# Performance work log

Hardware: AMD Instinct MI355X
Metric: run time of the kernel (lower is better)

The kernel has to match this reference:

```python
import jax, jax.numpy as jnp
import numpy as np

DIM, HEADS, K = 64, 4, 7
HEAD_DIM = DIM // HEADS
SCALE = HEAD_DIM ** -0.5  # qk_scale = head_dim ** -0.5


def setup_inputs() -> dict:
    key = jax.random.key(0)
    ks = jax.random.split(key, 6)
    B, H, W, SH, SW = 1, 192, 192, 12, 12
    x = jax.random.normal(ks[0], (B, DIM, H, W), dtype=jnp.float32)
    # soft pixel->superpixel association probabilities in [0,1)
    sims = jax.random.uniform(ks[1], (B, H, W, SH, SW), dtype=jnp.float32)
    s = DIM ** -0.5
    w_q = jax.random.normal(ks[2], (DIM, DIM), dtype=jnp.float32) * s
    w_k = jax.random.normal(ks[3], (DIM, DIM), dtype=jnp.float32) * s
    w_v = jax.random.normal(ks[4], (DIM, DIM), dtype=jnp.float32) * s
    w_proj = jax.random.normal(ks[5], (DIM, DIM), dtype=jnp.float32) * s
    return {"x": x, "sims": sims, "w_q": w_q, "w_k": w_k, "w_v": w_v, "w_proj": w_proj}


def _forward(x, sims, w_q, w_k, w_v, w_proj):
    B, C, H, W = x.shape
    SH, SW = sims.shape[-2:]
    h, d = HEADS, C // HEADS
    xf = jnp.transpose(x, (0, 2, 3, 1))                 # [B,H,W,C]
    q = (xf @ w_q).reshape(B, H, W, h, d)
    k = (xf @ w_k).reshape(B, H, W, h, d)
    v = (xf @ w_v).reshape(B, H, W, h, d)
    # NATTEN-style clamped neighborhood window starts
    sy = jnp.clip(jnp.arange(H) - K // 2, 0, H - K)     # [H]
    sx = jnp.clip(jnp.arange(W) - K // 2, 0, W - K)     # [W]
    # get_indices: nearest-interp of superpixel label grid -> hard cell per pixel
    si = (jnp.arange(H) * SH) // H                      # [H]
    sj = (jnp.arange(W) * SW) // W                      # [W]
    logits, masks = [], []
    for ky in range(K):                                  # fixed small kernel loop
        ny = sy + ky
        for kx in range(K):
            nx = sx + kx
            k_n = k[:, ny][:, :, nx]                    # [B,H,W,h,d] gathered neighbor keys
            logits.append(jnp.einsum('byxhd,byxhd->bhyx', q, k_n))
            # prob. neighbor pixel j belongs to query pixel i's superpixel cell
            masks.append(sims[:, ny[:, None], nx[None, :], si[:, None], sj[None, :]])  # [B,H,W]
    logits = jnp.stack(logits, -1)                      # [B,h,H,W,K*K]
    mask = jnp.stack(masks, -1)[:, None]                # [B,1,H,W,K*K]
    attn = jax.nn.softmax(SCALE * logits * mask, axis=-1)
    attn_m = attn * mask                                # soft-mask weighted aggregation
    out = jnp.zeros((B, h, H, W, d), x.dtype)
    o = 0
    for ky in range(K):
        ny = sy + ky
        for kx in range(K):
            nx = sx + kx
            v_n = jnp.transpose(v[:, ny][:, :, nx], (0, 3, 1, 2, 4))  # [B,h,H,W,d]
            out = out + attn_m[..., o, None] * v_n
            o += 1
    out = jnp.transpose(out, (0, 2, 3, 1, 4)).reshape(B, H, W, C)
    out = out @ w_proj
    return jnp.transpose(out, (0, 3, 1, 2))             # back to NCHW


def reference(x, sims, w_q, w_k, w_v, w_proj):
    return _forward(x, sims, w_q, w_k, w_v, w_proj)
```

## Files before the change

### kernel.cpp

```cpp
#include <hip/hip_runtime.h>
#include <math.h>

#define HH 192
#define WW 192
#define NPIX (HH * WW)
#define SCALE 0.25f

#define HLY 14
#define HLX 10
#define NH  (HLY * HLX)
#define REG2 (NH * 8 + 4)

typedef __attribute__((ext_vector_type(8))) _Float16 f16x8;
typedef __attribute__((ext_vector_type(2))) _Float16 f16x2;
typedef __attribute__((ext_vector_type(4))) float f32x4;

#if __has_builtin(__builtin_amdgcn_fdot2)
#define FDOT2(a, b, c) __builtin_amdgcn_fdot2((a), (b), (c), false)
#else
#define FDOT2(a, b, c) fmaf((float)(a)[0], (float)(b)[0], \
                            fmaf((float)(a)[1], (float)(b)[1], (c)))
#endif

static __device__ __forceinline__ f16x2 u2h(unsigned int u)
{
    f16x2 r; __builtin_memcpy(&r, &u, 4); return r;
}

static __device__ __forceinline__ short f16s(float f)
{
    _Float16 h = (_Float16)f;
    short s; __builtin_memcpy(&s, &h, 2); return s;
}

static __device__ __forceinline__ unsigned int pack_f16(float a, float b)
{
    unsigned short ul = (unsigned short)f16s(a);
    unsigned short uh = (unsigned short)f16s(b);
    return ((unsigned int)uh << 16) | ul;
}

__global__ __launch_bounds__(256) void qkv_mfma(
    const float* __restrict__ x,
    const float* __restrict__ wq, const float* __restrict__ wk,
    const float* __restrict__ wv, const float* __restrict__ wp,
    unsigned int* __restrict__ qg, unsigned int* __restrict__ kg,
    unsigned int* __restrict__ vg, short* __restrict__ wT)
{
    const int t = threadIdx.x;

    if (blockIdx.x == NPIX / 64) {
        #pragma unroll
        for (int i = 0; i < 16; ++i) {
            const int idx = i * 256 + t;
            const int n = idx >> 6, k = idx & 63;
            wT[(192 + n) * 64 + k] = f16s(wp[k * 64 + n]);
        }
        return;
    }

    __shared__ short lds[(64 + 192) * 72];
    short* xT = lds;
    short* wTs = lds + 64 * 72;
    const int px0 = blockIdx.x * 64;

    #pragma unroll
    for (int r = 0; r < 16; ++r) {
        const int idx = r * 256 + t;
        const int cin = idx >> 6, pxl = idx & 63;
        xT[pxl * 72 + cin] = f16s(x[(size_t)cin * NPIX + px0 + pxl]);
    }
    #pragma unroll
    for (int m = 0; m < 3; ++m) {
        const float* ws = (m == 0) ? wq : (m == 1) ? wk : wv;
        #pragma unroll
        for (int r = 0; r < 16; ++r) {
            const int idx = r * 256 + t;
            const int k = idx >> 6, n = idx & 63;
            wTs[(m * 64 + n) * 72 + k] = f16s(ws[k * 64 + n]);
        }
    }
    __syncthreads();

    const int lane = t & 63;
    const int wid  = t >> 6;
    const int l15  = lane & 15;
    const int kg4  = lane >> 4;

    f32x4 acc[12];
    #pragma unroll
    for (int nt = 0; nt < 12; ++nt) acc[nt] = (f32x4){0.f, 0.f, 0.f, 0.f};

    #pragma unroll
    for (int ks = 0; ks < 2; ++ks) {
        const f16x8 a = *reinterpret_cast<const f16x8*>(
            &xT[(wid * 16 + l15) * 72 + ks * 32 + kg4 * 8]);
        #pragma unroll
        for (int nt = 0; nt < 12; ++nt) {
            const f16x8 b = *reinterpret_cast<const f16x8*>(
                &wTs[(nt * 16 + l15) * 72 + ks * 32 + kg4 * 8]);
            acc[nt] = __builtin_amdgcn_mfma_f32_16x16x32_f16(a, b, acc[nt], 0, 0, 0);
        }
    }

    #pragma unroll
    for (int nt = 0; nt < 12; ++nt) {
        unsigned int* dst = (nt < 4) ? qg : (nt < 8) ? kg : vg;
        const int dwb = (nt & 3) * 8 + (l15 >> 1);
        #pragma unroll
        for (int r = 0; r < 4; ++r) {
            const float val = acc[nt][r];
            const float par = __shfl_xor(val, 1, 64);
            if (!(lane & 1)) {
                const int opx = px0 + wid * 16 + kg4 * 4 + r;
                dst[(size_t)opx * 32 + dwb] = pack_f16(val, par);
            }
        }
    }
}

#define NBR_STEP(HIDX)                                                        \
    {                                                                         \
        const int hidx_ = (HIDX);                                             \
        const uint4 ka = *reinterpret_cast<const uint4*>(kreg + hidx_ * 8);   \
        const uint4 k2 = *reinterpret_cast<const uint4*>(kreg + hidx_ * 8 + 4);\
        float da = FDOT2(u2h(ka.x), qv2[0], 0.f);                             \
        float db = FDOT2(u2h(ka.y), qv2[1], 0.f);                             \
        da = FDOT2(u2h(ka.z), qv2[2], da);                                    \
        db = FDOT2(u2h(ka.w), qv2[3], db);                                    \
        da = FDOT2(u2h(k2.x), qv2[4], da);                                    \
        db = FDOT2(u2h(k2.y), qv2[5], db);                                    \
        da = FDOT2(u2h(k2.z), qv2[6], da);                                    \
        db = FDOT2(u2h(k2.w), qv2[7], db);                                    \
        const float dot = da + db;                                            \
        const float m = sm[hidx_];                                            \
        const float pf = __expf(SCALE * dot * m) * 0.0625f;                   \
        S += pf;                                                              \
        const _Float16 pmh = (_Float16)(pf * m);                              \
        const f16x2 pm2 = {pmh, pmh};                                         \
        const uint4 va = *reinterpret_cast<const uint4*>(vreg + hidx_ * 8);   \
        const uint4 v2 = *reinterpret_cast<const uint4*>(vreg + hidx_ * 8 + 4);\
        acc2[0] = pm2 * u2h(va.x) + acc2[0];                                  \
        acc2[1] = pm2 * u2h(va.y) + acc2[1];                                  \
        acc2[2] = pm2 * u2h(va.z) + acc2[2];                                  \
        acc2[3] = pm2 * u2h(va.w) + acc2[3];                                  \
        acc2[4] = pm2 * u2h(v2.x) + acc2[4];                                  \
        acc2[5] = pm2 * u2h(v2.y) + acc2[5];                                  \
        acc2[6] = pm2 * u2h(v2.z) + acc2[6];                                  \
        acc2[7] = pm2 * u2h(v2.w) + acc2[7];                                  \
    }

__global__ __launch_bounds__(256) void attn_proj(
    const unsigned int* __restrict__ qg,
    const unsigned int* __restrict__ kg,
    const unsigned int* __restrict__ vg,
    const float* __restrict__ sims,
    const short* __restrict__ wT,
    float* __restrict__ out)
{
    __shared__ unsigned int smem[8 * REG2 + NH];

    const int bid = blockIdx.x;
    const int tl = (bid & 7) * 144 + (bid >> 3);
    const int ty = tl / 48, tx = tl - ty * 48;
    const int Y0 = ty * 8, X0 = tx * 4;
    int hy0 = Y0 - 3; hy0 = hy0 < 0 ? 0 : (hy0 > HH - HLY ? HH - HLY : hy0);
    int hx0 = X0 - 3; hx0 = hx0 < 0 ? 0 : (hx0 > WW - HLX ? WW - HLX : hx0);
    const int t = threadIdx.x;

    #pragma unroll
    for (int i = 0; i < 5; ++i) {
        const int idx = i * 256 + t;
        if (idx < NH * 8) {
            const int hidx = idx >> 3, u = idx & 7;
            const int r = hidx / HLX, c = hidx - r * HLX;
            const int np = (hy0 + r) * WW + hx0 + c;
            const int h = u >> 1, hf = u & 1;
            const size_t src = (size_t)np * 32 + u * 4;
            const uint4 kk = *reinterpret_cast<const uint4*>(kg + src);
            const uint4 vv = *reinterpret_cast<const uint4*>(vg + src);
            unsigned int* dk = smem + h * REG2 + hidx * 8 + hf * 4;
            *reinterpret_cast<uint4*>(dk) = kk;
            *reinterpret_cast<uint4*>(dk + 4 * REG2) = vv;
        }
    }
    if (t < NH) {
        const int r = t / HLX, c = t - r * HLX;
        const int np = (hy0 + r) * WW + hx0 + c;
        const int sbase = (Y0 >> 4) * 12 + (X0 >> 4);
        reinterpret_cast<float*>(smem)[8 * REG2 + t] = sims[np * 144 + sbase];
    }
    __syncthreads();

    const int half = t & 1, hl = (t >> 1) & 1, p = (t >> 2) & 31, hp = t >> 7;
    const int h = hp * 2 + hl;
    const int py = p >> 2, pxq = p & 3;
    const int y = Y0 + py, xq = X0 + pxq;
    int sy = y - 3;  sy = sy < 0 ? 0 : (sy > HH - 7 ? HH - 7 : sy);
    int sx = xq - 3; sx = sx < 0 ? 0 : (sx > WW - 7 ? WW - 7 : sx);
    const int wbase = (sy - hy0) * HLX + (sx - hx0);

    f16x2 qv2[8];
    {
        const unsigned int* qp = qg + (size_t)(y * WW + xq) * 32 + h * 8;
        const uint4 a = *reinterpret_cast<const uint4*>(qp);
        const uint4 b = *reinterpret_cast<const uint4*>(qp + 4);
        qv2[0] = u2h(a.x); qv2[1] = u2h(a.y); qv2[2] = u2h(a.z); qv2[3] = u2h(a.w);
        qv2[4] = u2h(b.x); qv2[5] = u2h(b.y); qv2[6] = u2h(b.z); qv2[7] = u2h(b.w);
    }

    const unsigned int* kreg = smem + h * REG2;
    const unsigned int* vreg = smem + (4 + h) * REG2;
    const float* sm = reinterpret_cast<const float*>(smem + 8 * REG2);

    float S = 0.f;
    f16x2 acc2[8];
    #pragma unroll
    for (int d = 0; d < 8; ++d) acc2[d] = (f16x2){(_Float16)0.f, (_Float16)0.f};

    #pragma unroll
    for (int i = 0; i < 24; ++i) {
        const int nn = 2 * i + half;
        const int ky = (nn * 37) >> 8;
        const int kx = nn - 7 * ky;
        NBR_STEP(wbase + ky * HLX + kx);
    }
    if (half == 0) {
        NBR_STEP(wbase + 6 * HLX + 6);
    }

    const float S2 = S + __shfl_xor(S, 1, 64);
    float lo[8], hi[8];
    #pragma unroll
    for (int j = 0; j < 8; ++j) {
        lo[j] = (float)acc2[j >> 1][j & 1];
        hi[j] = (float)acc2[4 + (j >> 1)][j & 1];
    }
    #pragma unroll
    for (int j = 0; j < 8; ++j) {
        lo[j] += __shfl_xor(lo[j], 1, 64);
        hi[j] += __shfl_xor(hi[j], 1, 64);
    }
    const float inv = 1.f / S2;
    float o[8];
    #pragma unroll
    for (int j = 0; j < 8; ++j) o[j] = ((half == 0) ? lo[j] : hi[j]) * inv;

    __syncthreads();
    {
        short* A_lds = reinterpret_cast<short*>(smem);
        const uint4 w4 = make_uint4(pack_f16(o[0], o[1]), pack_f16(o[2], o[3]),
                                    pack_f16(o[4], o[5]), pack_f16(o[6], o[7]));
        *reinterpret_cast<uint4*>(&A_lds[p * 72 + h * 16 + half * 8]) = w4;
    }
    __syncthreads();

    const short* A_lds = reinterpret_cast<const short*>(smem);
    const int lane = t & 63;
    const int w    = t >> 6;
    const int mt   = w & 1;
    const int np2  = w >> 1;
    const int l15  = lane & 15;
    const int kg4  = lane >> 4;

    f16x8 afrag[2];
    #pragma unroll
    for (int ks = 0; ks < 2; ++ks)
        afrag[ks] = *reinterpret_cast<const f16x8*>(
            &A_lds[(mt * 16 + l15) * 72 + ks * 32 + kg4 * 8]);

    #pragma unroll
    for (int nt2 = 0; nt2 < 2; ++nt2) {
        const int nt = np2 * 2 + nt2;
        const int n = nt * 16 + l15;
        f32x4 pacc = (f32x4){0.f, 0.f, 0.f, 0.f};
        #pragma unroll
        for (int ks = 0; ks < 2; ++ks) {
            const f16x8 b = *reinterpret_cast<const f16x8*>(
                &wT[(192 + n) * 64 + ks * 32 + kg4 * 8]);
            pacc = __builtin_amdgcn_mfma_f32_16x16x32_f16(afrag[ks], b, pacc, 0, 0, 0);
        }
        const int pr = mt * 16 + kg4 * 4;
        const int gy = Y0 + (pr >> 2);
        *reinterpret_cast<float4*>(out + (size_t)n * NPIX + gy * WW + X0) =
            make_float4(pacc[0], pacc[1], pacc[2], pacc[3]);
    }
}

extern "C" void kernel_launch(void* const* d_in, const int* in_sizes, int n_in,
                              void* d_out, int out_size, void* d_ws, size_t ws_size,
                              hipStream_t stream)
{
    const float* x    = (const float*)d_in[0];
    const float* sims = (const float*)d_in[1];
    const float* wq   = (const float*)d_in[2];
    const float* wk   = (const float*)d_in[3];
    const float* wv   = (const float*)d_in[4];
    const float* wp   = (const float*)d_in[5];
    float* out = (float*)d_out;

    unsigned int* qg = (unsigned int*)d_ws;
    unsigned int* kg = qg + (size_t)NPIX * 32;
    unsigned int* vg = kg + (size_t)NPIX * 32;
    short* wT = (short*)(vg + (size_t)NPIX * 32);

    qkv_mfma<<<NPIX / 64 + 1, 256, 0, stream>>>(x, wq, wk, wv, wp, qg, kg, vg, wT);
    attn_proj<<<1152, 256, 0, stream>>>(qg, kg, vg, sims, wT, out);
}
```

Measured before the change: 38.48 us.

## Compute neighborhood attention with MFMA over dense halo tile using transpose LDS reads

Replaces the per-thread fdot2 neighborhood loop with MFMA matrix products. Each wave, one per head, computes QK scores for 16 queries against a 10x16 halo of keys and applies PV with another MFMA, masking out-of-window entries. The tile shape changes to 4x8, V is staged in LDS and read with ds_read_b64_tr_b16, K is loaded straight from global, and exp is folded into exp2 with a prescaled mask. This trades redundant dense computation over about 160 slots per query against the 49 needed for far higher matrix throughput. It also depends on inline asm and a hand-placed waitcnt.

```diff
diff --git a/kernel.cpp b/kernel.cpp
--- a/kernel.cpp
+++ b/kernel.cpp
@@ -5,27 +5,24 @@
 #define WW 192
 #define NPIX (HH * WW)
 #define SCALE 0.25f
-
-#define HLY 14
-#define HLX 10
-#define NH  (HLY * HLX)
-#define REG2 (NH * 8 + 4)
+#define C1 0.36067376f
+
+#define HR 10
+#define HC 14
+#define NSLOT 160
+#define VOFF 160
 
 typedef __attribute__((ext_vector_type(8))) _Float16 f16x8;
-typedef __attribute__((ext_vector_type(2))) _Float16 f16x2;
+typedef __attribute__((ext_vector_type(4))) _Float16 f16x4;
 typedef __attribute__((ext_vector_type(4))) float f32x4;
 
-#if __has_builtin(__builtin_amdgcn_fdot2)
-#define FDOT2(a, b, c) __builtin_amdgcn_fdot2((a), (b), (c), false)
+#if __has_builtin(__builtin_amdgcn_exp2f)
+#define EXP2(x) __builtin_amdgcn_exp2f(x)
 #else
-#define FDOT2(a, b, c) fmaf((float)(a)[0], (float)(b)[0], \
-                            fmaf((float)(a)[1], (float)(b)[1], (c)))
+#define EXP2(x) exp2f(x)
 #endif
 
-static __device__ __forceinline__ f16x2 u2h(unsigned int u)
-{
-    f16x2 r; __builtin_memcpy(&r, &u, 4); return r;
-}
+#define MFMA16(a, b, c) __builtin_amdgcn_mfma_f32_16x16x16f16((a), (b), (c), 0, 0, 0)
 
 static __device__ __forceinline__ short f16s(float f)
 {
@@ -119,37 +116,6 @@
     }
 }
 
-#define NBR_STEP(HIDX)                                                        \
-    {                                                                         \
-        const int hidx_ = (HIDX);                                             \
-        const uint4 ka = *reinterpret_cast<const uint4*>(kreg + hidx_ * 8);   \
-        const uint4 k2 = *reinterpret_cast<const uint4*>(kreg + hidx_ * 8 + 4);\
-        float da = FDOT2(u2h(ka.x), qv2[0], 0.f);                             \
-        float db = FDOT2(u2h(ka.y), qv2[1], 0.f);                             \
-        da = FDOT2(u2h(ka.z), qv2[2], da);                                    \
-        db = FDOT2(u2h(ka.w), qv2[3], db);                                    \
-        da = FDOT2(u2h(k2.x), qv2[4], da);                                    \
-        db = FDOT2(u2h(k2.y), qv2[5], db);                                    \
-        da = FDOT2(u2h(k2.z), qv2[6], da);                                    \
-        db = FDOT2(u2h(k2.w), qv2[7], db);                                    \
-        const float dot = da + db;                                            \
-        const float m = sm[hidx_];                                            \
-        const float pf = __expf(SCALE * dot * m) * 0.0625f;                   \
-        S += pf;                                                              \
-        const _Float16 pmh = (_Float16)(pf * m);                              \
-        const f16x2 pm2 = {pmh, pmh};                                         \
-        const uint4 va = *reinterpret_cast<const uint4*>(vreg + hidx_ * 8);   \
-        const uint4 v2 = *reinterpret_cast<const uint4*>(vreg + hidx_ * 8 + 4);\
-        acc2[0] = pm2 * u2h(va.x) + acc2[0];                                  \
-        acc2[1] = pm2 * u2h(va.y) + acc2[1];                                  \
-        acc2[2] = pm2 * u2h(va.z) + acc2[2];                                  \
-        acc2[3] = pm2 * u2h(va.w) + acc2[3];                                  \
-        acc2[4] = pm2 * u2h(v2.x) + acc2[4];                                  \
-        acc2[5] = pm2 * u2h(v2.y) + acc2[5];                                  \
-        acc2[6] = pm2 * u2h(v2.z) + acc2[6];                                  \
-        acc2[7] = pm2 * u2h(v2.w) + acc2[7];                                  \
-    }
-
 __global__ __launch_bounds__(256) void attn_proj(
     const unsigned int* __restrict__ qg,
     const unsigned int* __restrict__ kg,
@@ -158,110 +124,144 @@
     const short* __restrict__ wT,
     float* __restrict__ out)
 {
-    __shared__ unsigned int smem[8 * REG2 + NH];
+    __shared__ unsigned int smem[VOFF + 4 * 160 * 8];
 
     const int bid = blockIdx.x;
     const int tl = (bid & 7) * 144 + (bid >> 3);
-    const int ty = tl / 48, tx = tl - ty * 48;
-    const int Y0 = ty * 8, X0 = tx * 4;
-    int hy0 = Y0 - 3; hy0 = hy0 < 0 ? 0 : (hy0 > HH - HLY ? HH - HLY : hy0);
-    int hx0 = X0 - 3; hx0 = hx0 < 0 ? 0 : (hx0 > WW - HLX ? WW - HLX : hx0);
+    const int ty = tl / 24, tx = tl - ty * 24;
+    const int Y0 = ty * 4, X0 = tx * 8;
+    int hy0 = Y0 - 3; hy0 = hy0 < 0 ? 0 : (hy0 > HH - HR ? HH - HR : hy0);
+    int hx0 = X0 - 3; hx0 = hx0 < 0 ? 0 : (hx0 > WW - HC ? WW - HC : hx0);
     const int t = threadIdx.x;
 
     #pragma unroll
     for (int i = 0; i < 5; ++i) {
         const int idx = i * 256 + t;
-        if (idx < NH * 8) {
-            const int hidx = idx >> 3, u = idx & 7;
-            const int r = hidx / HLX, c = hidx - r * HLX;
-            const int np = (hy0 + r) * WW + hx0 + c;
-            const int h = u >> 1, hf = u & 1;
-            const size_t src = (size_t)np * 32 + u * 4;
-            const uint4 kk = *reinterpret_cast<const uint4*>(kg + src);
-            const uint4 vv = *reinterpret_cast<const uint4*>(vg + src);
-            unsigned int* dk = smem + h * REG2 + hidx * 8 + hf * 4;
-            *reinterpret_cast<uint4*>(dk) = kk;
-            *reinterpret_cast<uint4*>(dk + 4 * REG2) = vv;
-        }
-    }
-    if (t < NH) {
-        const int r = t / HLX, c = t - r * HLX;
-        const int np = (hy0 + r) * WW + hx0 + c;
-        const int sbase = (Y0 >> 4) * 12 + (X0 >> 4);
-        reinterpret_cast<float*>(smem)[8 * REG2 + t] = sims[np * 144 + sbase];
+        const int n = idx >> 3, u = idx & 7;
+        const int ry = n >> 4, cx = n & 15;
+        uint4 vv = make_uint4(0u, 0u, 0u, 0u);
+        if (cx < HC) {
+            const int np = (hy0 + ry) * WW + hx0 + cx;
+            vv = *reinterpret_cast<const uint4*>(vg + (size_t)np * 32 + u * 4);
+        }
+        const int h = u >> 1, hf = u & 1;
+        *reinterpret_cast<uint4*>(smem + VOFF + h * 1280 + n * 8 + hf * 4) = vv;
+    }
+    if (t < NSLOT) {
+        const int ry = t >> 4, cx = t & 15;
+        float m = 0.f;
+        if (cx < HC) {
+            const int np = (hy0 + ry) * WW + hx0 + cx;
+            const int sbase = (Y0 >> 4) * 12 + (X0 >> 4);
+            m = sims[np * 144 + sbase];
+        }
+        reinterpret_cast<float*>(smem)[t] = m * C1;
     }
     __syncthreads();
 
-    const int half = t & 1, hl = (t >> 1) & 1, p = (t >> 2) & 31, hp = t >> 7;
-    const int h = hp * 2 + hl;
-    const int py = p >> 2, pxq = p & 3;
-    const int y = Y0 + py, xq = X0 + pxq;
-    int sy = y - 3;  sy = sy < 0 ? 0 : (sy > HH - 7 ? HH - 7 : sy);
-    int sx = xq - 3; sx = sx < 0 ? 0 : (sx > WW - 7 ? WW - 7 : sx);
-    const int wbase = (sy - hy0) * HLX + (sx - hx0);
-
-    f16x2 qv2[8];
-    {
-        const unsigned int* qp = qg + (size_t)(y * WW + xq) * 32 + h * 8;
-        const uint4 a = *reinterpret_cast<const uint4*>(qp);
-        const uint4 b = *reinterpret_cast<const uint4*>(qp + 4);
-        qv2[0] = u2h(a.x); qv2[1] = u2h(a.y); qv2[2] = u2h(a.z); qv2[3] = u2h(a.w);
-        qv2[4] = u2h(b.x); qv2[5] = u2h(b.y); qv2[6] = u2h(b.z); qv2[7] = u2h(b.w);
-    }
-
-    const unsigned int* kreg = smem + h * REG2;
-    const unsigned int* vreg = smem + (4 + h) * REG2;
-    const float* sm = reinterpret_cast<const float*>(smem + 8 * REG2);
-
-    float S = 0.f;
-    f16x2 acc2[8];
-    #pragma unroll
-    for (int d = 0; d < 8; ++d) acc2[d] = (f16x2){(_Float16)0.f, (_Float16)0.f};
-
-    #pragma unroll
-    for (int i = 0; i < 24; ++i) {
-        const int nn = 2 * i + half;
-        const int ky = (nn * 37) >> 8;
-        const int kx = nn - 7 * ky;
-        NBR_STEP(wbase + ky * HLX + kx);
-    }
-    if (half == 0) {
-        NBR_STEP(wbase + 6 * HLX + 6);
-    }
-
-    const float S2 = S + __shfl_xor(S, 1, 64);
-    float lo[8], hi[8];
-    #pragma unroll
-    for (int j = 0; j < 8; ++j) {
-        lo[j] = (float)acc2[j >> 1][j & 1];
-        hi[j] = (float)acc2[4 + (j >> 1)][j & 1];
-    }
-    #pragma unroll
-    for (int j = 0; j < 8; ++j) {
-        lo[j] += __shfl_xor(lo[j], 1, 64);
-        hi[j] += __shfl_xor(hi[j], 1, 64);
-    }
-    const float inv = 1.f / S2;
-    float o[8];
-    #pragma unroll
-    for (int j = 0; j < 8; ++j) o[j] = ((half == 0) ? lo[j] : hi[j]) * inv;
+    const int h    = t >> 6;
+    const int lane = t & 63;
+    const int l15  = lane & 15;
+    const int kg4  = lane >> 4;
+    const float* mC = reinterpret_cast<const float*>(smem);
+
+    const unsigned vbyte = (unsigned)(uintptr_t)smem + VOFF * 4
+                         + h * 5120 + lane * 8;
+    f16x4 vf[10];
+#define TRREAD(I, IMM) \
+    asm volatile("ds_read_b64_tr_b16 %0, %1 offset:" IMM \
+                 : "=v"(vf[I]) : "v"(vbyte))
+    TRREAD(0, "0");    TRREAD(1, "512");  TRREAD(2, "1024"); TRREAD(3, "1536");
+    TRREAD(4, "2048"); TRREAD(5, "2560"); TRREAD(6, "3072"); TRREAD(7, "3584");
+    TRREAD(8, "4096"); TRREAD(9, "4608");
+#undef TRREAD
+
+    const unsigned int* kgp = kg + (size_t)(hy0 * WW + hx0 + l15) * 32
+                            + h * 8 + kg4 * 2;
+    f16x4 kf[10];
+    #pragma unroll
+    for (int nt = 0; nt < 10; ++nt)
+        kf[nt] = *reinterpret_cast<const f16x4*>(kgp + (size_t)nt * (WW * 32));
+
+    f32x4 oacc[2];
+    float invq[2];
+    bool waited = false;
+
+    #pragma unroll
+    for (int qt = 0; qt < 2; ++qt) {
+        const int q = qt * 16 + l15;
+        const int qry = q >> 3, qcx = q & 7;
+        const int y = Y0 + qry, x = X0 + qcx;
+        int sy = y - 3; sy = sy < 0 ? 0 : (sy > HH - 7 ? HH - 7 : sy);
+        int sx = x - 3; sx = sx < 0 ? 0 : (sx > WW - 7 ? WW - 7 : sx);
+        const int wy = sy - hy0, wx = sx - hx0;
+
+        const f16x4 qb = *reinterpret_cast<const f16x4*>(
+            qg + (size_t)(y * WW + x) * 32 + h * 8 + kg4 * 2);
+
+        f32x4 s[10];
+        #pragma unroll
+        for (int nt = 0; nt < 10; ++nt)
+            s[nt] = MFMA16(kf[nt], qb, ((f32x4){0.f, 0.f, 0.f, 0.f}));
+
+        float vx[4];
+        #pragma unroll
+        for (int rr = 0; rr < 4; ++rr)
+            vx[rr] = ((unsigned)(kg4 * 4 + rr - wx) < 7u) ? 1.f : 0.f;
+
+        float Ss = 0.f;
+        f16x4 pt[10];
+        #pragma unroll
+        for (int nt = 0; nt < 10; ++nt) {
+            const f32x4 mcv = *reinterpret_cast<const f32x4*>(
+                mC + nt * 16 + kg4 * 4);
+            const float vy = ((unsigned)(nt - wy) < 7u) ? 1.f : 0.f;
+            float pf[4];
+            #pragma unroll
+            for (int e = 0; e < 4; ++e) {
+                const float u = s[nt][e] * mcv[e];
+                const float p = EXP2(u);
+                const float pv = p * vy * vx[e];
+                Ss += pv;
+                pf[e] = pv * mcv[e];
+            }
+            pt[nt] = (f16x4){(_Float16)pf[0], (_Float16)pf[1],
+                             (_Float16)pf[2], (_Float16)pf[3]};
+        }
+        Ss += __shfl_xor(Ss, 16, 64);
+        Ss += __shfl_xor(Ss, 32, 64);
+        invq[qt] = 1.f / (C1 * Ss);
+
+        if (!waited) {
+            asm volatile("s_waitcnt lgkmcnt(0)" ::: "memory");
+            __builtin_amdgcn_sched_barrier(0);
+            waited = true;
+        }
+        f32x4 o = (f32x4){0.f, 0.f, 0.f, 0.f};
+        #pragma unroll
+        for (int nt = 0; nt < 10; ++nt)
+            o = MFMA16(vf[nt], pt[nt], o);
+        oacc[qt] = o;
+    }
 
     __syncthreads();
     {
-        short* A_lds = reinterpret_cast<short*>(smem);
-        const uint4 w4 = make_uint4(pack_f16(o[0], o[1]), pack_f16(o[2], o[3]),
-                                    pack_f16(o[4], o[5]), pack_f16(o[6], o[7]));
-        *reinterpret_cast<uint4*>(&A_lds[p * 72 + h * 16 + half * 8]) = w4;
+        short* A = reinterpret_cast<short*>(smem);
+        #pragma unroll
+        for (int qt = 0; qt < 2; ++qt) {
+            const int q = qt * 16 + l15;
+            const float iv = invq[qt];
+            const f16x4 ov = (f16x4){
+                (_Float16)(oacc[qt][0] * iv), (_Float16)(oacc[qt][1] * iv),
+                (_Float16)(oacc[qt][2] * iv), (_Float16)(oacc[qt][3] * iv)};
+            *reinterpret_cast<f16x4*>(&A[q * 72 + h * 16 + kg4 * 4]) = ov;
+        }
     }
     __syncthreads();
 
     const short* A_lds = reinterpret_cast<const short*>(smem);
-    const int lane = t & 63;
-    const int w    = t >> 6;
-    const int mt   = w & 1;
-    const int np2  = w >> 1;
-    const int l15  = lane & 15;
-    const int kg4  = lane >> 4;
+    const int mt  = h & 1;
+    const int np2 = h >> 1;
 
     f16x8 afrag[2];
     #pragma unroll
@@ -271,8 +271,7 @@
 
     #pragma unroll
     for (int nt2 = 0; nt2 < 2; ++nt2) {
-        const int nt = np2 * 2 + nt2;
-        const int n = nt * 16 + l15;
+        const int n = (np2 * 2 + nt2) * 16 + l15;
         f32x4 pacc = (f32x4){0.f, 0.f, 0.f, 0.f};
         #pragma unroll
         for (int ks = 0; ks < 2; ++ks) {
@@ -281,8 +280,8 @@
             pacc = __builtin_amdgcn_mfma_f32_16x16x32_f16(afrag[ks], b, pacc, 0, 0, 0);
         }
         const int pr = mt * 16 + kg4 * 4;
-        const int gy = Y0 + (pr >> 2);
-        *reinterpret_cast<float4*>(out + (size_t)n * NPIX + gy * WW + X0) =
+        const int gy = Y0 + (pr >> 3), gx = X0 + (pr & 7);
+        *reinterpret_cast<float4*>(out + (size_t)n * NPIX + gy * WW + gx) =
             make_float4(pacc[0], pacc[1], pacc[2], pacc[3]);
     }
 }
```

Measured after the change: 40.57 us. 5.4% more time.
